# Performance work log

Measured on AMD Instinct MI355X. Metric: run time of the kernel, lower is better.

Reference implementation:

```python
import jax, jax.numpy as jnp
from jax import lax
import numpy as np

I, H, C2 = 14, 64, 2  # input_size, hidden_size, num_classes
B, T = 8192, 256


def _lstm_layer(x_seq, w_ih, w_hh, b_ih, b_hh):
    # x_seq: [T, B, in]; w_ih: [4H, in]; w_hh: [4H, H]; gate order: i, f, g, o (PyTorch)
    Bb = x_seq.shape[1]
    Hh = w_hh.shape[1]
    # precompute input projections for all timesteps in one GEMM
    xg = jnp.einsum('tbi,gi->tbg', x_seq, w_ih) + b_ih + b_hh  # [T, B, 4H]

    def step(carry, xg_t):
        h, c = carry
        g = xg_t + h @ w_hh.T  # [B, 4H]
        i_g, f_g, g_g, o_g = jnp.split(g, 4, axis=-1)
        i_g = jax.nn.sigmoid(i_g)
        f_g = jax.nn.sigmoid(f_g)
        g_g = jnp.tanh(g_g)
        o_g = jax.nn.sigmoid(o_g)
        c = f_g * c + i_g * g_g
        h = o_g * jnp.tanh(c)
        return (h, c), h

    h0 = jnp.zeros((Bb, Hh), x_seq.dtype)
    (_, _), hs = lax.scan(step, (h0, h0), xg)
    return hs  # [T, B, H]


def setup_inputs() -> dict:
    key = jax.random.key(0)
    ks = jax.random.split(key, 13)
    s_ih0 = 1.0 / np.sqrt(H)
    inp = {
        'x': jax.random.normal(ks[0], (B, T, I), dtype=jnp.float32),
        'w_ih0': jax.random.uniform(ks[1], (4 * H, I), jnp.float32, -s_ih0, s_ih0),
        'w_hh0': jax.random.uniform(ks[2], (4 * H, H), jnp.float32, -s_ih0, s_ih0),
        'b_ih0': jax.random.uniform(ks[3], (4 * H,), jnp.float32, -s_ih0, s_ih0),
        'b_hh0': jax.random.uniform(ks[4], (4 * H,), jnp.float32, -s_ih0, s_ih0),
        'w_ih1': jax.random.uniform(ks[5], (4 * H, H), jnp.float32, -s_ih0, s_ih0),
        'w_hh1': jax.random.uniform(ks[6], (4 * H, H), jnp.float32, -s_ih0, s_ih0),
        'b_ih1': jax.random.uniform(ks[7], (4 * H,), jnp.float32, -s_ih0, s_ih0),
        'b_hh1': jax.random.uniform(ks[8], (4 * H,), jnp.float32, -s_ih0, s_ih0),
        'w_fc1': jax.random.uniform(ks[9], (64, H), jnp.float32, -s_ih0, s_ih0),
        'b_fc1': jax.random.uniform(ks[10], (64,), jnp.float32, -s_ih0, s_ih0),
        'w_fc2': jax.random.uniform(ks[11], (C2, 64), jnp.float32, -1.0 / 8, 1.0 / 8),
        'b_fc2': jax.random.uniform(ks[12], (C2,), jnp.float32, -1.0 / 8, 1.0 / 8),
    }
    return inp


def reference(x, w_ih0, w_hh0, b_ih0, b_hh0, w_ih1, w_hh1, b_ih1, b_hh1, w_fc1, b_fc1, w_fc2, b_fc2):
    xt = jnp.transpose(x, (1, 0, 2))  # [T, B, I]
    h1 = _lstm_layer(xt, w_ih0, w_hh0, b_ih0, b_hh0)   # [T, B, H]
    # inter-layer dropout is identity in eval mode
    h2 = _lstm_layer(h1, w_ih1, w_hh1, b_ih1, b_hh1)   # [T, B, H]
    last = h2[-1]                                      # [B, H]
    z = jax.nn.relu(last @ w_fc1.T + b_fc1)            # dropout identity in eval
    return z @ w_fc2.T + b_fc2                         # [B, num_classes]
```

## Files before the change

### kernel.cpp

```cpp
#include <hip/hip_runtime.h>


#define TT 256
#define II 14
#define BB 16
#define NTHREADS 256
#define XP 40
#define HP 72
#define LOG2E 1.44269504088896340736f

typedef _Float16 f16x8 __attribute__((ext_vector_type(8)));
typedef _Float16 f16x4 __attribute__((ext_vector_type(4)));
typedef float f32x4 __attribute__((ext_vector_type(4)));

__device__ __forceinline__ f32x4 MFMA16(f16x8 a, f16x8 b, f32x4 c) {
  return __builtin_amdgcn_mfma_f32_16x16x32_f16(a, b, c, 0, 0, 0);
}

__device__ __forceinline__ float ex2(float x) {
#if __has_builtin(__builtin_amdgcn_exp2f)
  return __builtin_amdgcn_exp2f(x);
#else
  float r; asm("v_exp_f32 %0, %1" : "=v"(r) : "v"(x)); return r;
#endif
}
__device__ __forceinline__ float rcp_(float x) {
#if __has_builtin(__builtin_amdgcn_rcpf)
  return __builtin_amdgcn_rcpf(x);
#else
  float r; asm("v_rcp_f32 %0, %1" : "=v"(r) : "v"(x)); return r;
#endif
}

__device__ __forceinline__ f16x4 lstm_act(f32x4 si, f32x4 sf, f32x4 sg, f32x4 so,
                                          f32x4& cs) {
  f16x4 hp;
#pragma unroll
  for (int r = 0; r < 4; ++r) {
    const float ui = ex2(si[r]);
    const float uf = ex2(sf[r]);
    const float ug = ex2(sg[r]);
    const float uo = ex2(so[r]);
    const float fi = 1.0f + ui;
    const float ff = 1.0f + uf;
    const float fg = 1.0f + ug;
    const float pig = fi * fg;
    const float num = fmaf(cs[r], pig, (ug - 1.0f) * ff);
    const float c = num * rcp_(pig * ff);
    cs[r] = c;
    const float ut = ex2(2.0f * LOG2E * c);
    const float h = (ut - 1.0f) * rcp_((1.0f + uo) * (1.0f + ut));
    hp[r] = (_Float16)h;
  }
  return hp;
}

__global__ void __launch_bounds__(NTHREADS, 2) fused_lstm(
    const float* __restrict__ x,
    const float* __restrict__ w_ih0, const float* __restrict__ w_hh0,
    const float* __restrict__ b_ih0, const float* __restrict__ b_hh0,
    const float* __restrict__ w_ih1, const float* __restrict__ w_hh1,
    const float* __restrict__ b_ih1, const float* __restrict__ b_hh1,
    const float* __restrict__ w_fc1, const float* __restrict__ b_fc1,
    const float* __restrict__ w_fc2, const float* __restrict__ b_fc2,
    float* __restrict__ out) {
  __shared__ char smem[11776];

  const int tid = threadIdx.x;
  const int w = tid >> 6;
  const int l = tid & 63;
  const int row16 = l & 15;
  const int kblk = l >> 4;
  const int b0 = blockIdx.x * BB;

  f16x8 a_ih0[4], a_hh0[4][2], a_ih1[4][2], a_hh1[4][2];
#pragma unroll
  for (int gt = 0; gt < 4; ++gt) {
    const float sc = (gt == 2) ? (2.0f * LOG2E) : (-LOG2E);
    const int g = gt * 64 + w * 16 + row16;
    {
      f16x8 v;
#pragma unroll
      for (int j = 0; j < 8; ++j) {
        const int k = kblk * 8 + j;
        v[j] = (k < II) ? (_Float16)(w_ih0[g * II + k] * sc) : (_Float16)0.0f;
      }
      a_ih0[gt] = v;
    }
#pragma unroll
    for (int ks = 0; ks < 2; ++ks) {
      const int ko = ks * 32 + kblk * 8;
      f16x8 v0, v1, v2;
#pragma unroll
      for (int j = 0; j < 8; ++j) v0[j] = (_Float16)(w_hh0[g * 64 + ko + j] * sc);
#pragma unroll
      for (int j = 0; j < 8; ++j) v1[j] = (_Float16)(w_ih1[g * 64 + ko + j] * sc);
#pragma unroll
      for (int j = 0; j < 8; ++j) v2[j] = (_Float16)(w_hh1[g * 64 + ko + j] * sc);
      a_hh0[gt][ks] = v0;
      a_ih1[gt][ks] = v1;
      a_hh1[gt][ks] = v2;
    }
  }
  f32x4 bias0[4], bias1[4];
#pragma unroll
  for (int gt = 0; gt < 4; ++gt) {
    const float sc = (gt == 2) ? (2.0f * LOG2E) : (-LOG2E);
#pragma unroll
    for (int r = 0; r < 4; ++r) {
      const int g = gt * 64 + w * 16 + kblk * 4 + r;
      bias0[gt][r] = (b_ih0[g] + b_hh0[g]) * sc;
      bias1[gt][r] = (b_ih1[g] + b_hh1[g]) * sc;
    }
  }

  for (int i = tid; i < 11776 / 4; i += NTHREADS) ((int*)smem)[i] = 0;

  const int n0 = tid / II, k0 = tid - n0 * II;
  const bool hasx = tid < BB * II;
  const float* xp0 = x + (size_t)(b0 + (hasx ? n0 : 0)) * (TT * II) + k0;

  __syncthreads();
  if (hasx) *((_Float16*)(smem + 9216) + n0 * XP + k0) = (_Float16)xp0[0];
  __syncthreads();

  f32x4 c0s = {0.f, 0.f, 0.f, 0.f}, c1s = {0.f, 0.f, 0.f, 0.f};

  const int boff = row16 * HP + kblk * 8;
  const int woff = row16 * HP + w * 16 + kblk * 4;

  {
    const _Float16* xs = (const _Float16*)(smem + 9216);
    const _Float16* h0r = (const _Float16*)(smem + 4608 + 2304);
    f32x4 acc0[4];
#pragma unroll
    for (int gt = 0; gt < 4; ++gt) acc0[gt] = bias0[gt];
    const f16x8 bx = *(const f16x8*)(xs + row16 * XP + kblk * 8);
    const f16x8 bh0a = *(const f16x8*)(h0r + boff);
    const f16x8 bh0c = *(const f16x8*)(h0r + 32 + boff);
#pragma unroll
    for (int gt = 0; gt < 4; ++gt) {
      acc0[gt] = MFMA16(a_ih0[gt], bx, acc0[gt]);
      acc0[gt] = MFMA16(a_hh0[gt][0], bh0a, acc0[gt]);
      acc0[gt] = MFMA16(a_hh0[gt][1], bh0c, acc0[gt]);
    }
    float xn = hasx ? xp0[II] : 0.0f;
    const f16x4 h0p = lstm_act(acc0[0], acc0[1], acc0[2], acc0[3], c0s);
    *(f16x4*)((_Float16*)(smem + 4608) + woff) = h0p;
    if (hasx) *((_Float16*)(smem + 9216 + 1280) + n0 * XP + k0) = (_Float16)xn;
    __syncthreads();
  }

#pragma unroll 2
  for (int t = 1; t < TT; ++t) {
    const int pc = t & 1, pp = pc ^ 1;
    const _Float16* xs = (const _Float16*)(smem + 9216 + pc * 1280);
    const _Float16* h0r = (const _Float16*)(smem + 4608 + pp * 2304);
    const _Float16* h1r = (const _Float16*)(smem + pc * 2304);
    _Float16* h0w = (_Float16*)(smem + 4608 + pc * 2304);
    _Float16* h1w = (_Float16*)(smem + pp * 2304);
    _Float16* xsw = (_Float16*)(smem + 9216 + pp * 1280);

    const f16x8 bx = *(const f16x8*)(xs + row16 * XP + kblk * 8);
    const f16x8 bh0a = *(const f16x8*)(h0r + boff);
    const f16x8 bh0c = *(const f16x8*)(h0r + 32 + boff);
    const f16x8 bh1a = *(const f16x8*)(h1r + boff);
    const f16x8 bh1c = *(const f16x8*)(h1r + 32 + boff);
    f32x4 acc0[4], acc1[4];
#pragma unroll
    for (int gt = 0; gt < 4; ++gt) {
      acc0[gt] = bias0[gt];
      acc1[gt] = bias1[gt];
    }
#pragma unroll
    for (int gt = 0; gt < 4; ++gt) {
      acc0[gt] = MFMA16(a_ih0[gt], bx, acc0[gt]);
      acc0[gt] = MFMA16(a_hh0[gt][0], bh0a, acc0[gt]);
      acc0[gt] = MFMA16(a_hh0[gt][1], bh0c, acc0[gt]);
      acc1[gt] = MFMA16(a_ih1[gt][0], bh0a, acc1[gt]);
      acc1[gt] = MFMA16(a_ih1[gt][1], bh0c, acc1[gt]);
      acc1[gt] = MFMA16(a_hh1[gt][0], bh1a, acc1[gt]);
      acc1[gt] = MFMA16(a_hh1[gt][1], bh1c, acc1[gt]);
    }

    float xn = 0.0f;
    if (hasx && t + 1 < TT) xn = xp0[(size_t)(t + 1) * II];

    const f16x4 h0p = lstm_act(acc0[0], acc0[1], acc0[2], acc0[3], c0s);
    const f16x4 h1p = lstm_act(acc1[0], acc1[1], acc1[2], acc1[3], c1s);

    *(f16x4*)(h0w + woff) = h0p;
    *(f16x4*)(h1w + woff) = h1p;
    if (hasx && t + 1 < TT) xsw[n0 * XP + k0] = (_Float16)xn;
    __syncthreads();
  }

  {
    const _Float16* h0r = (const _Float16*)(smem + 4608 + 2304);
    const _Float16* h1r = (const _Float16*)(smem);
    _Float16* h1w = (_Float16*)(smem + 2304);
    f32x4 acc1[4];
#pragma unroll
    for (int gt = 0; gt < 4; ++gt) acc1[gt] = bias1[gt];
    const f16x8 bh0a = *(const f16x8*)(h0r + boff);
    const f16x8 bh0c = *(const f16x8*)(h0r + 32 + boff);
    const f16x8 bh1a = *(const f16x8*)(h1r + boff);
    const f16x8 bh1c = *(const f16x8*)(h1r + 32 + boff);
#pragma unroll
    for (int gt = 0; gt < 4; ++gt) {
      acc1[gt] = MFMA16(a_ih1[gt][0], bh0a, acc1[gt]);
      acc1[gt] = MFMA16(a_ih1[gt][1], bh0c, acc1[gt]);
      acc1[gt] = MFMA16(a_hh1[gt][0], bh1a, acc1[gt]);
      acc1[gt] = MFMA16(a_hh1[gt][1], bh1c, acc1[gt]);
    }
    const f16x4 h1p = lstm_act(acc1[0], acc1[1], acc1[2], acc1[3], c1s);
    *(f16x4*)(h1w + woff) = h1p;
    __syncthreads();
  }

  const _Float16* h1f = (const _Float16*)(smem + 2304);
  float* zbuf = (float*)(smem + 4608);
  float4 w1r[16];
#pragma unroll
  for (int k4 = 0; k4 < 16; ++k4) w1r[k4] = *(const float4*)(w_fc1 + l * 64 + k4 * 4);
  const float b1l = b_fc1[l];
#pragma unroll
  for (int bi = 0; bi < 4; ++bi) {
    const int n = w * 4 + bi;
    float s = b1l;
#pragma unroll
    for (int k4 = 0; k4 < 16; ++k4) {
      const float4 wv = w1r[k4];
      s = fmaf((float)h1f[n * HP + k4 * 4 + 0], wv.x, s);
      s = fmaf((float)h1f[n * HP + k4 * 4 + 1], wv.y, s);
      s = fmaf((float)h1f[n * HP + k4 * 4 + 2], wv.z, s);
      s = fmaf((float)h1f[n * HP + k4 * 4 + 3], wv.w, s);
    }
    zbuf[n * 64 + l] = fmaxf(s, 0.0f);
  }
  __syncthreads();
  if (tid < 2 * BB) {
    const int n = tid >> 1, cc = tid & 1;
    float s = b_fc2[cc];
    for (int j = 0; j < 64; ++j) s = fmaf(w_fc2[cc * 64 + j], zbuf[n * 64 + j], s);
    out[(size_t)(b0 + n) * 2 + cc] = s;
  }
}

extern "C" void kernel_launch(void* const* d_in, const int* in_sizes, int n_in,
                              void* d_out, int out_size, void* d_ws, size_t ws_size,
                              hipStream_t stream) {
  (void)in_sizes; (void)n_in; (void)d_ws; (void)ws_size; (void)out_size;
  const float* x = (const float*)d_in[0];
  const float* w_ih0 = (const float*)d_in[1];
  const float* w_hh0 = (const float*)d_in[2];
  const float* b_ih0 = (const float*)d_in[3];
  const float* b_hh0 = (const float*)d_in[4];
  const float* w_ih1 = (const float*)d_in[5];
  const float* w_hh1 = (const float*)d_in[6];
  const float* b_ih1 = (const float*)d_in[7];
  const float* b_hh1 = (const float*)d_in[8];
  const float* w_fc1 = (const float*)d_in[9];
  const float* b_fc1 = (const float*)d_in[10];
  const float* w_fc2 = (const float*)d_in[11];
  const float* b_fc2 = (const float*)d_in[12];

  fused_lstm<<<dim3(8192 / BB), dim3(NTHREADS), 0, stream>>>(
      x, w_ih0, w_hh0, b_ih0, b_hh0, w_ih1, w_hh1, b_ih1, b_hh1,
      w_fc1, b_fc1, w_fc2, b_fc2, (float*)d_out);
}
```

Measured before the change: 360.6 us.

## Split LSTM layers across two wave groups in a 512-thread block

Doubles the block to 512 threads and gives layer 0 and layer 1 to separate groups of four waves, so each wave runs only one layer's MFMAs and activations per timestep. Each wave now holds half the weight registers, which shortens the per-step critical path and may allow more waves per CU. The cost is imbalance: the layer-0 group does fewer MFMAs than the layer-1 group and waits at the barrier, and each block-wide barrier now spans eight waves.

Result: faster. 337.5 us (-6.4%).

```diff
diff --git a/kernel.cpp b/kernel.cpp
--- a/kernel.cpp
+++ b/kernel.cpp
@@ -4,7 +4,7 @@
 #define TT 256
 #define II 14
 #define BB 16
-#define NTHREADS 256
+#define NTHREADS 512
 #define XP 40
 #define HP 72
 #define LOG2E 1.44269504088896340736f
@@ -55,7 +55,7 @@
   return hp;
 }
 
-__global__ void __launch_bounds__(NTHREADS, 2) fused_lstm(
+__global__ void __launch_bounds__(NTHREADS, 4) fused_lstm(
     const float* __restrict__ x,
     const float* __restrict__ w_ih0, const float* __restrict__ w_hh0,
     const float* __restrict__ b_ih0, const float* __restrict__ b_hh0,
@@ -67,50 +67,55 @@
   __shared__ char smem[11776];
 
   const int tid = threadIdx.x;
-  const int w = tid >> 6;
+  const int wv = tid >> 6;
+  const int grp = wv >> 2;
+  const int wl = wv & 3;
   const int l = tid & 63;
   const int row16 = l & 15;
   const int kblk = l >> 4;
+
   const int b0 = blockIdx.x * BB;
 
-  f16x8 a_ih0[4], a_hh0[4][2], a_ih1[4][2], a_hh1[4][2];
+  f16x8 wIn[4][2], wRec[4][2];
+  f32x4 bias[4];
 #pragma unroll
   for (int gt = 0; gt < 4; ++gt) {
     const float sc = (gt == 2) ? (2.0f * LOG2E) : (-LOG2E);
-    const int g = gt * 64 + w * 16 + row16;
-    {
+    const int g = gt * 64 + wl * 16 + row16;
+    if (grp == 0) {
       f16x8 v;
 #pragma unroll
       for (int j = 0; j < 8; ++j) {
         const int k = kblk * 8 + j;
         v[j] = (k < II) ? (_Float16)(w_ih0[g * II + k] * sc) : (_Float16)0.0f;
       }
-      a_ih0[gt] = v;
-    }
-#pragma unroll
-    for (int ks = 0; ks < 2; ++ks) {
-      const int ko = ks * 32 + kblk * 8;
-      f16x8 v0, v1, v2;
-#pragma unroll
-      for (int j = 0; j < 8; ++j) v0[j] = (_Float16)(w_hh0[g * 64 + ko + j] * sc);
-#pragma unroll
-      for (int j = 0; j < 8; ++j) v1[j] = (_Float16)(w_ih1[g * 64 + ko + j] * sc);
-#pragma unroll
-      for (int j = 0; j < 8; ++j) v2[j] = (_Float16)(w_hh1[g * 64 + ko + j] * sc);
-      a_hh0[gt][ks] = v0;
-      a_ih1[gt][ks] = v1;
-      a_hh1[gt][ks] = v2;
-    }
-  }
-  f32x4 bias0[4], bias1[4];
-#pragma unroll
-  for (int gt = 0; gt < 4; ++gt) {
-    const float sc = (gt == 2) ? (2.0f * LOG2E) : (-LOG2E);
+      wIn[gt][0] = v;
+#pragma unroll
+      for (int ks = 0; ks < 2; ++ks) {
+        const int ko = ks * 32 + kblk * 8;
+        f16x8 vr;
+#pragma unroll
+        for (int j = 0; j < 8; ++j) vr[j] = (_Float16)(w_hh0[g * 64 + ko + j] * sc);
+        wRec[gt][ks] = vr;
+      }
+    } else {
+#pragma unroll
+      for (int ks = 0; ks < 2; ++ks) {
+        const int ko = ks * 32 + kblk * 8;
+        f16x8 vi, vr;
+#pragma unroll
+        for (int j = 0; j < 8; ++j) vi[j] = (_Float16)(w_ih1[g * 64 + ko + j] * sc);
+#pragma unroll
+        for (int j = 0; j < 8; ++j) vr[j] = (_Float16)(w_hh1[g * 64 + ko + j] * sc);
+        wIn[gt][ks] = vi;
+        wRec[gt][ks] = vr;
+      }
+    }
+    const int gb = gt * 64 + wl * 16 + kblk * 4;
 #pragma unroll
     for (int r = 0; r < 4; ++r) {
-      const int g = gt * 64 + w * 16 + kblk * 4 + r;
-      bias0[gt][r] = (b_ih0[g] + b_hh0[g]) * sc;
-      bias1[gt][r] = (b_ih1[g] + b_hh1[g]) * sc;
+      bias[gt][r] = (grp == 0) ? (b_ih0[gb + r] + b_hh0[gb + r]) * sc
+                               : (b_ih1[gb + r] + b_hh1[gb + r]) * sc;
     }
   }
 
@@ -120,123 +125,123 @@
   const bool hasx = tid < BB * II;
   const float* xp0 = x + (size_t)(b0 + (hasx ? n0 : 0)) * (TT * II) + k0;
 
-  __syncthreads();
-  if (hasx) *((_Float16*)(smem + 9216) + n0 * XP + k0) = (_Float16)xp0[0];
-  __syncthreads();
-
-  f32x4 c0s = {0.f, 0.f, 0.f, 0.f}, c1s = {0.f, 0.f, 0.f, 0.f};
+  _Float16* H1 = (_Float16*)smem;
+  _Float16* H0 = (_Float16*)(smem + 4608);
+  _Float16* XS = (_Float16*)(smem + 9216);
+
+  __syncthreads();
+  if (hasx) XS[n0 * XP + k0] = (_Float16)xp0[0];
+  __syncthreads();
+
+  f32x4 cs = {0.f, 0.f, 0.f, 0.f};
 
   const int boff = row16 * HP + kblk * 8;
-  const int woff = row16 * HP + w * 16 + kblk * 4;
-
-  {
-    const _Float16* xs = (const _Float16*)(smem + 9216);
-    const _Float16* h0r = (const _Float16*)(smem + 4608 + 2304);
-    f32x4 acc0[4];
-#pragma unroll
-    for (int gt = 0; gt < 4; ++gt) acc0[gt] = bias0[gt];
-    const f16x8 bx = *(const f16x8*)(xs + row16 * XP + kblk * 8);
-    const f16x8 bh0a = *(const f16x8*)(h0r + boff);
-    const f16x8 bh0c = *(const f16x8*)(h0r + 32 + boff);
+  const int woff = row16 * HP + wl * 16 + kblk * 4;
+
+  if (grp == 0) {
+    f32x4 acc[4];
+#pragma unroll
+    for (int gt = 0; gt < 4; ++gt) acc[gt] = bias[gt];
+    const f16x8 bx = *(const f16x8*)(XS + row16 * XP + kblk * 8);
+    const f16x8 bhA = *(const f16x8*)(H0 + 1152 + boff);
+    const f16x8 bhB = *(const f16x8*)(H0 + 1152 + 32 + boff);
 #pragma unroll
     for (int gt = 0; gt < 4; ++gt) {
-      acc0[gt] = MFMA16(a_ih0[gt], bx, acc0[gt]);
-      acc0[gt] = MFMA16(a_hh0[gt][0], bh0a, acc0[gt]);
-      acc0[gt] = MFMA16(a_hh0[gt][1], bh0c, acc0[gt]);
-    }
-    float xn = hasx ? xp0[II] : 0.0f;
-    const f16x4 h0p = lstm_act(acc0[0], acc0[1], acc0[2], acc0[3], c0s);
-    *(f16x4*)((_Float16*)(smem + 4608) + woff) = h0p;
-    if (hasx) *((_Float16*)(smem + 9216 + 1280) + n0 * XP + k0) = (_Float16)xn;
-    __syncthreads();
-  }
+      acc[gt] = MFMA16(wIn[gt][0], bx, acc[gt]);
+      acc[gt] = MFMA16(wRec[gt][0], bhA, acc[gt]);
+      acc[gt] = MFMA16(wRec[gt][1], bhB, acc[gt]);
+    }
+    const float xn = hasx ? (float)xp0[II] : 0.0f;
+    const f16x4 hp = lstm_act(acc[0], acc[1], acc[2], acc[3], cs);
+    *(f16x4*)(H0 + woff) = hp;
+    if (hasx) XS[640 + n0 * XP + k0] = (_Float16)xn;
+  }
+  __syncthreads();
 
 #pragma unroll 2
   for (int t = 1; t < TT; ++t) {
     const int pc = t & 1, pp = pc ^ 1;
-    const _Float16* xs = (const _Float16*)(smem + 9216 + pc * 1280);
-    const _Float16* h0r = (const _Float16*)(smem + 4608 + pp * 2304);
-    const _Float16* h1r = (const _Float16*)(smem + pc * 2304);
-    _Float16* h0w = (_Float16*)(smem + 4608 + pc * 2304);
-    _Float16* h1w = (_Float16*)(smem + pp * 2304);
-    _Float16* xsw = (_Float16*)(smem + 9216 + pp * 1280);
-
-    const f16x8 bx = *(const f16x8*)(xs + row16 * XP + kblk * 8);
-    const f16x8 bh0a = *(const f16x8*)(h0r + boff);
-    const f16x8 bh0c = *(const f16x8*)(h0r + 32 + boff);
-    const f16x8 bh1a = *(const f16x8*)(h1r + boff);
-    const f16x8 bh1c = *(const f16x8*)(h1r + 32 + boff);
-    f32x4 acc0[4], acc1[4];
+    if (grp == 0) {
+      f32x4 acc[4];
+#pragma unroll
+      for (int gt = 0; gt < 4; ++gt) acc[gt] = bias[gt];
+      const f16x8 bx = *(const f16x8*)(XS + pc * 640 + row16 * XP + kblk * 8);
+      const f16x8 bhA = *(const f16x8*)(H0 + pp * 1152 + boff);
+      const f16x8 bhB = *(const f16x8*)(H0 + pp * 1152 + 32 + boff);
+#pragma unroll
+      for (int gt = 0; gt < 4; ++gt) {
+        acc[gt] = MFMA16(wIn[gt][0], bx, acc[gt]);
+        acc[gt] = MFMA16(wRec[gt][0], bhA, acc[gt]);
+        acc[gt] = MFMA16(wRec[gt][1], bhB, acc[gt]);
+      }
+      float xn = 0.0f;
+      if (hasx && t + 1 < TT) xn = xp0[(size_t)(t + 1) * II];
+      const f16x4 hp = lstm_act(acc[0], acc[1], acc[2], acc[3], cs);
+      *(f16x4*)(H0 + pc * 1152 + woff) = hp;
+      if (hasx && t + 1 < TT) XS[pp * 640 + n0 * XP + k0] = (_Float16)xn;
+    } else {
+      f32x4 acc[4];
+#pragma unroll
+      for (int gt = 0; gt < 4; ++gt) acc[gt] = bias[gt];
+      const f16x8 bgA = *(const f16x8*)(H0 + pp * 1152 + boff);
+      const f16x8 bgB = *(const f16x8*)(H0 + pp * 1152 + 32 + boff);
+      const f16x8 bhA = *(const f16x8*)(H1 + pc * 1152 + boff);
+      const f16x8 bhB = *(const f16x8*)(H1 + pc * 1152 + 32 + boff);
+#pragma unroll
+      for (int gt = 0; gt < 4; ++gt) {
+        acc[gt] = MFMA16(wIn[gt][0], bgA, acc[gt]);
+        acc[gt] = MFMA16(wIn[gt][1], bgB, acc[gt]);
+        acc[gt] = MFMA16(wRec[gt][0], bhA, acc[gt]);
+        acc[gt] = MFMA16(wRec[gt][1], bhB, acc[gt]);
+      }
+      const f16x4 hp = lstm_act(acc[0], acc[1], acc[2], acc[3], cs);
+      *(f16x4*)(H1 + pp * 1152 + woff) = hp;
+    }
+    __syncthreads();
+  }
+
+  if (grp == 1) {
+    f32x4 acc[4];
+#pragma unroll
+    for (int gt = 0; gt < 4; ++gt) acc[gt] = bias[gt];
+    const f16x8 bgA = *(const f16x8*)(H0 + 1152 + boff);
+    const f16x8 bgB = *(const f16x8*)(H0 + 1152 + 32 + boff);
+    const f16x8 bhA = *(const f16x8*)(H1 + boff);
+    const f16x8 bhB = *(const f16x8*)(H1 + 32 + boff);
 #pragma unroll
     for (int gt = 0; gt < 4; ++gt) {
-      acc0[gt] = bias0[gt];
-      acc1[gt] = bias1[gt];
-    }
-#pragma unroll
-    for (int gt = 0; gt < 4; ++gt) {
-      acc0[gt] = MFMA16(a_ih0[gt], bx, acc0[gt]);
-      acc0[gt] = MFMA16(a_hh0[gt][0], bh0a, acc0[gt]);
-      acc0[gt] = MFMA16(a_hh0[gt][1], bh0c, acc0[gt]);
-      acc1[gt] = MFMA16(a_ih1[gt][0], bh0a, acc1[gt]);
-      acc1[gt] = MFMA16(a_ih1[gt][1], bh0c, acc1[gt]);
-      acc1[gt] = MFMA16(a_hh1[gt][0], bh1a, acc1[gt]);
-      acc1[gt] = MFMA16(a_hh1[gt][1], bh1c, acc1[gt]);
-    }
-
-    float xn = 0.0f;
-    if (hasx && t + 1 < TT) xn = xp0[(size_t)(t + 1) * II];
-
-    const f16x4 h0p = lstm_act(acc0[0], acc0[1], acc0[2], acc0[3], c0s);
-    const f16x4 h1p = lstm_act(acc1[0], acc1[1], acc1[2], acc1[3], c1s);
-
-    *(f16x4*)(h0w + woff) = h0p;
-    *(f16x4*)(h1w + woff) = h1p;
-    if (hasx && t + 1 < TT) xsw[n0 * XP + k0] = (_Float16)xn;
-    __syncthreads();
-  }
-
-  {
-    const _Float16* h0r = (const _Float16*)(smem + 4608 + 2304);
-    const _Float16* h1r = (const _Float16*)(smem);
-    _Float16* h1w = (_Float16*)(smem + 2304);
-    f32x4 acc1[4];
-#pragma unroll
-    for (int gt = 0; gt < 4; ++gt) acc1[gt] = bias1[gt];
-    const f16x8 bh0a = *(const f16x8*)(h0r + boff);
-    const f16x8 bh0c = *(const f16x8*)(h0r + 32 + boff);
-    const f16x8 bh1a = *(const f16x8*)(h1r + boff);
-    const f16x8 bh1c = *(const f16x8*)(h1r + 32 + boff);
-#pragma unroll
-    for (int gt = 0; gt < 4; ++gt) {
-      acc1[gt] = MFMA16(a_ih1[gt][0], bh0a, acc1[gt]);
-      acc1[gt] = MFMA16(a_ih1[gt][1], bh0c, acc1[gt]);
-      acc1[gt] = MFMA16(a_hh1[gt][0], bh1a, acc1[gt]);
-      acc1[gt] = MFMA16(a_hh1[gt][1], bh1c, acc1[gt]);
-    }
-    const f16x4 h1p = lstm_act(acc1[0], acc1[1], acc1[2], acc1[3], c1s);
-    *(f16x4*)(h1w + woff) = h1p;
-    __syncthreads();
-  }
+      acc[gt] = MFMA16(wIn[gt][0], bgA, acc[gt]);
+      acc[gt] = MFMA16(wIn[gt][1], bgB, acc[gt]);
+      acc[gt] = MFMA16(wRec[gt][0], bhA, acc[gt]);
+      acc[gt] = MFMA16(wRec[gt][1], bhB, acc[gt]);
+    }
+    const f16x4 hp = lstm_act(acc[0], acc[1], acc[2], acc[3], cs);
+    *(f16x4*)(H1 + 1152 + woff) = hp;
+  }
+  __syncthreads();
 
   const _Float16* h1f = (const _Float16*)(smem + 2304);
   float* zbuf = (float*)(smem + 4608);
-  float4 w1r[16];
-#pragma unroll
-  for (int k4 = 0; k4 < 16; ++k4) w1r[k4] = *(const float4*)(w_fc1 + l * 64 + k4 * 4);
-  const float b1l = b_fc1[l];
-#pragma unroll
-  for (int bi = 0; bi < 4; ++bi) {
-    const int n = w * 4 + bi;
-    float s = b1l;
-#pragma unroll
-    for (int k4 = 0; k4 < 16; ++k4) {
-      const float4 wv = w1r[k4];
-      s = fmaf((float)h1f[n * HP + k4 * 4 + 0], wv.x, s);
-      s = fmaf((float)h1f[n * HP + k4 * 4 + 1], wv.y, s);
-      s = fmaf((float)h1f[n * HP + k4 * 4 + 2], wv.z, s);
-      s = fmaf((float)h1f[n * HP + k4 * 4 + 3], wv.w, s);
-    }
-    zbuf[n * 64 + l] = fmaxf(s, 0.0f);
+  {
+    float4 w1r[16];
+#pragma unroll
+    for (int k4 = 0; k4 < 16; ++k4)
+      w1r[k4] = *(const float4*)(w_fc1 + l * 64 + k4 * 4);
+    const float b1l = b_fc1[l];
+#pragma unroll
+    for (int bi = 0; bi < 2; ++bi) {
+      const int n = wv * 2 + bi;
+      float s = b1l;
+#pragma unroll
+      for (int k4 = 0; k4 < 16; ++k4) {
+        const float4 wq = w1r[k4];
+        s = fmaf((float)h1f[n * HP + k4 * 4 + 0], wq.x, s);
+        s = fmaf((float)h1f[n * HP + k4 * 4 + 1], wq.y, s);
+        s = fmaf((float)h1f[n * HP + k4 * 4 + 2], wq.z, s);
+        s = fmaf((float)h1f[n * HP + k4 * 4 + 3], wq.w, s);
+      }
+      zbuf[n * 64 + l] = fmaxf(s, 0.0f);
+    }
   }
   __syncthreads();
   if (tid < 2 * BB) {
```
